# Optimization experiments

Measured on AMD Instinct MI355X. Metric: run time of the kernel, lower is better.

## Reference

```python
import jax, jax.numpy as jnp
import numpy as np

B, S, T = 4, 1024, 1024
HID, ATT, NH = 1024, 1024, 16
HD = ATT // NH  # head size 64


def setup_inputs() -> dict:
    key = jax.random.key(0)
    ks = jax.random.split(key, 12)
    sc = 1.0 / np.sqrt(HID)
    return {
        "src": jax.random.normal(ks[0], (B, S, HID), jnp.float32),
        "tgt": jax.random.normal(ks[1], (B, T, HID), jnp.float32),
        "src_mask": jax.random.randint(ks[2], (B, S), 0, 2) > 0,
        "tgt_mask": jax.random.randint(ks[3], (B, T), 0, 2) > 0,
        "qw": jax.random.normal(ks[4], (ATT, HID), jnp.float32) * sc,
        "qb": jnp.zeros((ATT,), jnp.float32),
        "kw": jax.random.normal(ks[5], (ATT, HID), jnp.float32) * sc,
        "kb": jnp.zeros((ATT,), jnp.float32),
        "vw": jax.random.normal(ks[6], (ATT, HID), jnp.float32) * sc,
        "vb": jnp.zeros((ATT,), jnp.float32),
        "ow": jax.random.normal(ks[7], (HID, ATT), jnp.float32) * (1.0 / np.sqrt(ATT)),
        "ob": jnp.zeros((HID,), jnp.float32),
    }


def _heads(x, w, b, L):
    # x:[B,L,HID] -> [B,NH,L,HD]
    return (x @ w.T + b).reshape(B, L, NH, HD).transpose(0, 2, 1, 3)


def reference(src, tgt, src_mask, tgt_mask, qw, qb, kw, kb, vw, vb, ow, ob):
    q = _heads(src, qw, qb, S)
    k = _heads(tgt, kw, kb, T)
    v_src = _heads(src, vw, vb, S)
    v_tgt = _heads(tgt, vw, vb, T)

    attn = jnp.einsum("bhsd,bhtd->bhst", q, k) / np.sqrt(HD)  # shared scores

    sm = src_mask[:, None, :, None].astype(attn.dtype)  # [B,1,S,1]
    tm = tgt_mask[:, None, None, :].astype(attn.dtype)  # [B,1,1,T]
    NEG = 100000.0
    attn_src = attn * sm - NEG * (1.0 - sm)
    attn_tgt = attn * tm - NEG * (1.0 - tm)

    p_src = jax.nn.softmax(attn_src, axis=-1)                        # [B,H,S,T]
    p_tgt = jax.nn.softmax(attn_tgt.swapaxes(-1, -2), axis=-1)       # [B,H,T,S]

    o_src = jnp.einsum("bhst,bhtd->bhsd", p_src, v_tgt)
    o_tgt = jnp.einsum("bhts,bhsd->bhtd", p_tgt, v_src)

    o_src = o_src.transpose(0, 2, 1, 3).reshape(B, S, ATT) @ ow.T + ob
    o_tgt = o_tgt.transpose(0, 2, 1, 3).reshape(B, T, ATT) @ ow.T + ob
    return (o_src, o_tgt)
```

## Files before the change

kernel.cpp:

```cpp
#include <hip/hip_runtime.h>
#include <stdint.h>

typedef _Float16 f16;
typedef _Float16 f16x8 __attribute__((ext_vector_type(8)));
typedef _Float16 f16x4 __attribute__((ext_vector_type(4)));
typedef float    f32x4 __attribute__((ext_vector_type(4)));

#define MFMA_F16(A, B, C) __builtin_amdgcn_mfma_f32_16x16x32_f16((A), (B), (C), 0, 0, 0)

__device__ __forceinline__ void gload_lds16(const void* g, void* l) {
  __builtin_amdgcn_global_load_lds((const __attribute__((address_space(1))) void*)g,
                                   (__attribute__((address_space(3))) void*)l, 16, 0, 0);
}

__global__ void cvt_f32_f16(const float* __restrict__ s0, const float* __restrict__ s1,
                            const float* __restrict__ s2, const float* __restrict__ s3,
                            const float* __restrict__ s4, const float* __restrict__ s5,
                            f16* __restrict__ d0, f16* __restrict__ d1, f16* __restrict__ d2,
                            f16* __restrict__ d3, f16* __restrict__ d4, f16* __restrict__ d5) {
  const float* sp; f16* dp; int n4;
  switch (blockIdx.y) {
    case 0:  sp = s0; dp = d0; n4 = (4096 * 1024) / 4; break;
    case 1:  sp = s1; dp = d1; n4 = (4096 * 1024) / 4; break;
    case 2:  sp = s2; dp = d2; n4 = (1024 * 1024) / 4; break;
    case 3:  sp = s3; dp = d3; n4 = (1024 * 1024) / 4; break;
    case 4:  sp = s4; dp = d4; n4 = (1024 * 1024) / 4; break;
    default: sp = s5; dp = d5; n4 = (1024 * 1024) / 4; break;
  }
  int stride = gridDim.x * blockDim.x;
  for (int i = blockIdx.x * blockDim.x + threadIdx.x; i < n4; i += stride) {
    f32x4 v = *(const f32x4*)(sp + (size_t)i * 4);
    f16x4 h;
    h[0] = (f16)v[0]; h[1] = (f16)v[1]; h[2] = (f16)v[2]; h[3] = (f16)v[3];
    *(f16x4*)(dp + (size_t)i * 4) = h;
  }
}

__device__ __forceinline__ void gemm_core_k1024(const f16* __restrict__ A, const f16* __restrict__ W,
                                                f16* lA, f16* lB, f32x4 (&acc)[4][4],
                                                int row0, int col0) {
  const int tid = threadIdx.x;
  const int lane = tid & 63;
  const int w = tid >> 6;
  const int g = lane >> 4, c = lane & 15;
  const int wr = (w >> 1) * 64, wc = (w & 1) * 64;

  int sr[2], scol[2];
#pragma unroll
  for (int p = 0; p < 2; ++p) {
    int slot = p * 256 + tid;
    int r = slot >> 2, sph = slot & 3;
    sr[p] = r;
    scol[p] = (sph ^ ((r >> 1) & 3)) * 8;
  }
  const f16* Abase = A + (size_t)row0 * 1024;
  const f16* Wbase = W + (size_t)col0 * 1024;

  for (int k0 = 0; k0 < 1024; k0 += 32) {
    __syncthreads();
#pragma unroll
    for (int p = 0; p < 2; ++p) {
      gload_lds16(Abase + (size_t)sr[p] * 1024 + k0 + scol[p], lA + (p * 256 + w * 64) * 8);
      gload_lds16(Wbase + (size_t)sr[p] * 1024 + k0 + scol[p], lB + (p * 256 + w * 64) * 8);
    }
    __syncthreads();
    f16x8 af[4], bf[4];
#pragma unroll
    for (int m = 0; m < 4; ++m) {
      int r = wr + m * 16 + c;
      af[m] = *(const f16x8*)(lA + r * 32 + (g ^ ((r >> 1) & 3)) * 8);
    }
#pragma unroll
    for (int n = 0; n < 4; ++n) {
      int r = wc + n * 16 + c;
      bf[n] = *(const f16x8*)(lB + r * 32 + (g ^ ((r >> 1) & 3)) * 8);
    }
#pragma unroll
    for (int m = 0; m < 4; ++m)
#pragma unroll
      for (int n = 0; n < 4; ++n)
        acc[m][n] = MFMA_F16(af[m], bf[n], acc[m][n]);
  }
}

__global__ __launch_bounds__(256, 2) void proj_gemm(
    const f16* __restrict__ src16, const f16* __restrict__ tgt16,
    const f16* __restrict__ qw16, const f16* __restrict__ kw16, const f16* __restrict__ vw16,
    const float* __restrict__ qb, const float* __restrict__ kb, const float* __restrict__ vb,
    f16* __restrict__ q16, f16* __restrict__ k16, f16* __restrict__ vtS, f16* __restrict__ vtT) {
  __shared__ f16 lA[128 * 32];
  __shared__ f16 lB[128 * 32];
  const int z = blockIdx.z;
  const f16* A = (z & 1) ? tgt16 : src16;
  const f16* W = (z == 0) ? qw16 : (z == 1) ? kw16 : vw16;
  const float* bias = (z == 0) ? qb : (z == 1) ? kb : vb;
  const int row0 = blockIdx.y * 128;
  const int col0 = blockIdx.x * 128;
  f32x4 acc[4][4] = {};
  gemm_core_k1024(A, W, lA, lB, acc, row0, col0);

  const int lane = threadIdx.x & 63;
  const int w = threadIdx.x >> 6;
  const int g = lane >> 4, c = lane & 15;
  const int wr = (w >> 1) * 64, wc = (w & 1) * 64;

  if (z < 2) {
    f16* O = (z == 0) ? q16 : k16;
#pragma unroll
    for (int n = 0; n < 4; ++n) {
      int colg = col0 + wc + n * 16 + c;
      float bv = bias[colg];
#pragma unroll
      for (int m = 0; m < 4; ++m) {
        int rb = row0 + wr + m * 16 + g * 4;
#pragma unroll
        for (int r = 0; r < 4; ++r)
          O[(size_t)(rb + r) * 1024 + colg] = (f16)(acc[m][n][r] + bv);
      }
    }
  } else {
    f16* O = (z == 2) ? vtS : vtT;
#pragma unroll
    for (int n = 0; n < 4; ++n) {
      int colg = col0 + wc + n * 16 + c;
      float bv = bias[colg];
#pragma unroll
      for (int m = 0; m < 4; ++m) {
        int row = row0 + wr + m * 16 + g * 4;
        int bb = row >> 10, t = row & 1023;
        int tl = t & 63;
        int tp = (t & ~63) + (tl & 32) + ((tl & 12) << 1) + ((tl & 16) >> 2) + (tl & 3);
        f16x4 pk;
#pragma unroll
        for (int r = 0; r < 4; ++r) pk[r] = (f16)(acc[m][n][r] + bv);
        *(f16x4*)(O + ((size_t)(bb << 10) + colg) * 1024 + tp) = pk;
      }
    }
  }
}

__global__ __launch_bounds__(256, 2) void out_gemm(
    const f16* __restrict__ opre, const f16* __restrict__ ow16,
    const float* __restrict__ ob, float* __restrict__ out) {
  __shared__ f16 lA[128 * 32];
  __shared__ f16 lB[128 * 32];
  const int row0 = blockIdx.y * 128;
  const int col0 = blockIdx.x * 128;
  f32x4 acc[4][4] = {};
  gemm_core_k1024(opre, ow16, lA, lB, acc, row0, col0);
  const int lane = threadIdx.x & 63;
  const int w = threadIdx.x >> 6;
  const int g = lane >> 4, c = lane & 15;
  const int wr = (w >> 1) * 64, wc = (w & 1) * 64;
#pragma unroll
  for (int n = 0; n < 4; ++n) {
    int colg = col0 + wc + n * 16 + c;
    float bv = ob[colg];
#pragma unroll
    for (int m = 0; m < 4; ++m) {
      int rb = row0 + wr + m * 16 + g * 4;
#pragma unroll
      for (int r = 0; r < 4; ++r)
        out[(size_t)(rb + r) * 1024 + colg] = acc[m][n][r] + bv;
    }
  }
}

__global__ __launch_bounds__(256, 3) void attn_fwd(
    const f16* __restrict__ q16, const f16* __restrict__ k16,
    const f16* __restrict__ vtS, const f16* __restrict__ vtT,
    const int* __restrict__ smask, const int* __restrict__ tmask,
    f16* __restrict__ opre) {
  const int bid = blockIdx.x;
  const int xcd = bid & 7;
  const int idx = bid >> 3;
  const int bhp = xcd * 16 + (idx >> 3);
  const int qblk = idx & 7;
  const int pass = bhp >> 6;
  const int bh = bhp & 63;
  const int b = bh >> 4, h = bh & 15;

  const f16* Q  = pass ? k16 : q16;
  const f16* Kt = pass ? q16 : k16;
  const f16* VT = pass ? vtS : vtT;
  const int* qmask = pass ? tmask : smask;
  const int outRowOff = pass ? 4096 : 0;

  const int tid = threadIdx.x;
  const int lane = tid & 63, wv = tid >> 6;
  const int g = lane >> 4, c = lane & 15;
  const int qrow0 = qblk * 128 + wv * 32;

  __shared__ f16 lK[2][64 * 64];
  __shared__ f16 lV[2][64 * 64];

  const size_t kbase = (size_t)b * (1024 * 1024) + h * 64;
  const size_t vbase = (size_t)bh * (64 * 1024);

  const float SC2 = 0.18033688f;
  f16x8 qf[2][2];
#pragma unroll
  for (int m = 0; m < 2; ++m) {
    f16 sh = (f16)(qmask[b * 1024 + qrow0 + m * 16 + c] ? SC2 : 0.0f);
#pragma unroll
    for (int kc = 0; kc < 2; ++kc) {
      f16x8 v = *(const f16x8*)(Q + ((size_t)(b * 1024 + qrow0 + m * 16 + c)) * 1024 + h * 64 + kc * 32 + g * 8);
#pragma unroll
      for (int j = 0; j < 8; ++j) v[j] *= sh;
      qf[m][kc] = v;
    }
  }

  auto STAGE = [&](int nb, int t0) {
#pragma unroll
    for (int i = 0; i < 2; ++i) {
      int p = i * 256 + tid;
      int row = p >> 3;
      int u = (p & 7) ^ (row & 7);
      gload_lds16(Kt + kbase + (size_t)(t0 + row) * 1024 + u * 8, &lK[nb][(i * 256 + wv * 64) * 8]);
      gload_lds16(VT + vbase + (size_t)row * 1024 + t0 + u * 8, &lV[nb][(i * 256 + wv * 64) * 8]);
    }
  };

  f32x4 accO[2][4] = {};
  float lpart[2] = {0.0f, 0.0f};

  STAGE(0, 0);

  for (int tt = 0; tt < 16; ++tt) {
    asm volatile("s_waitcnt vmcnt(0)" ::: "memory");
    __builtin_amdgcn_s_barrier();
    __builtin_amdgcn_sched_barrier(0);
    if (tt < 15) STAGE((tt + 1) & 1, (tt + 1) * 64);
    const f16* curK = lK[tt & 1];
    const f16* curV = lV[tt & 1];

    f16x8 kf[4][2];
#pragma unroll
    for (int n = 0; n < 4; ++n) {
      int row = n * 16 + c;
#pragma unroll
      for (int kc = 0; kc < 2; ++kc)
        kf[n][kc] = *(const f16x8*)(curK + row * 64 + (((kc * 4 + g) ^ (row & 7)) * 8));
    }

    f16x8 vf[4][2];
#pragma unroll
    for (int nd = 0; nd < 4; ++nd) {
      int row = nd * 16 + c;
#pragma unroll
      for (int kc = 0; kc < 2; ++kc)
        vf[nd][kc] = *(const f16x8*)(curV + row * 64 + (((kc * 4 + g) ^ (row & 7)) * 8));
    }

    f32x4 sc[2][4];
#pragma unroll
    for (int m = 0; m < 2; ++m)
#pragma unroll
      for (int n = 0; n < 4; ++n) {
        f32x4 z = {0.0f, 0.0f, 0.0f, 0.0f};
        z = MFMA_F16(kf[n][0], qf[m][0], z);
        sc[m][n] = MFMA_F16(kf[n][1], qf[m][1], z);
      }

    f16x8 pa[2][2];
#pragma unroll
    for (int m = 0; m < 2; ++m) {
      float e[16];
#pragma unroll
      for (int n = 0; n < 4; ++n)
#pragma unroll
        for (int r = 0; r < 4; ++r) e[n * 4 + r] = __builtin_amdgcn_exp2f(sc[m][n][r]);
      float s8[8];
#pragma unroll
      for (int i = 0; i < 8; ++i) s8[i] = e[i] + e[i + 8];
      float s4[4];
#pragma unroll
      for (int i = 0; i < 4; ++i) s4[i] = s8[i] + s8[i + 4];
      lpart[m] += (s4[0] + s4[1]) + (s4[2] + s4[3]);
#pragma unroll
      for (int kc = 0; kc < 2; ++kc) {
        f16x8 p8;
#pragma unroll
        for (int j = 0; j < 8; ++j) p8[j] = (f16)e[8 * kc + j];
        pa[m][kc] = p8;
      }
    }

#pragma unroll
    for (int m = 0; m < 2; ++m)
#pragma unroll
      for (int nd = 0; nd < 4; ++nd) {
        accO[m][nd] = MFMA_F16(pa[m][0], vf[nd][0], accO[m][nd]);
        accO[m][nd] = MFMA_F16(pa[m][1], vf[nd][1], accO[m][nd]);
      }
  }

#pragma unroll
  for (int m = 0; m < 2; ++m) {
    float ls = lpart[m];
    ls += __shfl_xor(ls, 16);
    ls += __shfl_xor(ls, 32);
#pragma unroll
    for (int r = 0; r < 4; ++r) {
      float lr = __shfl(ls, 20 * g + r);
      float inv = 1.0f / lr;
      size_t orow = (size_t)(outRowOff + b * 1024 + qrow0 + m * 16 + 4 * g + r);
#pragma unroll
      for (int nd = 0; nd < 4; ++nd)
        opre[orow * 1024 + h * 64 + nd * 16 + c] = (f16)(accO[m][nd][r] * inv);
    }
  }
}

extern "C" void kernel_launch(void* const* d_in, const int* in_sizes, int n_in,
                              void* d_out, int out_size, void* d_ws, size_t ws_size,
                              hipStream_t stream) {
  (void)in_sizes; (void)n_in; (void)out_size; (void)ws_size;
  const float* src = (const float*)d_in[0];
  const float* tgt = (const float*)d_in[1];
  const int*   smask = (const int*)d_in[2];
  const int*   tmask = (const int*)d_in[3];
  const float* qw = (const float*)d_in[4];
  const float* qb = (const float*)d_in[5];
  const float* kw = (const float*)d_in[6];
  const float* kb = (const float*)d_in[7];
  const float* vw = (const float*)d_in[8];
  const float* vb = (const float*)d_in[9];
  const float* ow = (const float*)d_in[10];
  const float* ob = (const float*)d_in[11];
  float* out = (float*)d_out;

  f16* wsp = (f16*)d_ws;
  const size_t M4 = (size_t)4096 * 1024;
  const size_t M1 = (size_t)1024 * 1024;
  f16* src16 = wsp;
  f16* tgt16 = src16 + M4;
  f16* qw16  = tgt16 + M4;
  f16* kw16  = qw16 + M1;
  f16* vw16  = kw16 + M1;
  f16* ow16  = vw16 + M1;
  f16* q16   = ow16 + M1;
  f16* k16   = q16 + M4;
  f16* vtS   = k16 + M4;
  f16* vtT   = vtS + M4;
  f16* opre  = wsp;

  cvt_f32_f16<<<dim3(512, 6), 256, 0, stream>>>(src, tgt, qw, kw, vw, ow,
                                                src16, tgt16, qw16, kw16, vw16, ow16);
  proj_gemm<<<dim3(8, 32, 4), 256, 0, stream>>>(src16, tgt16, qw16, kw16, vw16,
                                                qb, kb, vb, q16, k16, vtS, vtT);
  attn_fwd<<<dim3(1024), 256, 0, stream>>>(q16, k16, vtS, vtT, smask, tmask, opre);
  out_gemm<<<dim3(8, 64), 256, 0, stream>>>(opre, ow16, ob, out);
}
```

Before: 142.8 us.

## Double-buffer GEMM LDS tiles and remap blocks to XCDs for L2 reuse

The shared GEMM core now uses two LDS buffers and prefetches the next K tile while computing the current one, replacing the two-barrier-per-iteration single-buffer loop. The projection and output GEMMs switch to 1D grids whose block index is decoded so that blocks sharing an operand land on the same XCD, aiming for better L2 locality. This doubles LDS use per block, which may limit occupancy. The out_gemm mapping also carries dead, unused index computations.

After: 135.2 us. -5.3%, faster.

```diff
diff --git a/kernel.cpp b/kernel.cpp
--- a/kernel.cpp
+++ b/kernel.cpp
@@ -56,24 +56,37 @@
   const f16* Abase = A + (size_t)row0 * 1024;
   const f16* Wbase = W + (size_t)col0 * 1024;
 
-  for (int k0 = 0; k0 < 1024; k0 += 32) {
-    __syncthreads();
+  auto STAGE = [&](int nb, int k0) {
 #pragma unroll
     for (int p = 0; p < 2; ++p) {
-      gload_lds16(Abase + (size_t)sr[p] * 1024 + k0 + scol[p], lA + (p * 256 + w * 64) * 8);
-      gload_lds16(Wbase + (size_t)sr[p] * 1024 + k0 + scol[p], lB + (p * 256 + w * 64) * 8);
-    }
-    __syncthreads();
+      gload_lds16(Abase + (size_t)sr[p] * 1024 + k0 + scol[p],
+                  lA + nb * (128 * 32) + (p * 256 + w * 64) * 8);
+      gload_lds16(Wbase + (size_t)sr[p] * 1024 + k0 + scol[p],
+                  lB + nb * (128 * 32) + (p * 256 + w * 64) * 8);
+    }
+  };
+
+  STAGE(0, 0);
+
+  for (int kt = 0; kt < 32; ++kt) {
+    const int cur = kt & 1;
+    asm volatile("s_waitcnt vmcnt(0)" ::: "memory");
+    __builtin_amdgcn_s_barrier();
+    __builtin_amdgcn_sched_barrier(0);
+    if (kt < 31) STAGE(cur ^ 1, (kt + 1) * 32);
+
+    const f16* cA = lA + cur * (128 * 32);
+    const f16* cB = lB + cur * (128 * 32);
     f16x8 af[4], bf[4];
 #pragma unroll
     for (int m = 0; m < 4; ++m) {
       int r = wr + m * 16 + c;
-      af[m] = *(const f16x8*)(lA + r * 32 + (g ^ ((r >> 1) & 3)) * 8);
+      af[m] = *(const f16x8*)(cA + r * 32 + (g ^ ((r >> 1) & 3)) * 8);
     }
 #pragma unroll
     for (int n = 0; n < 4; ++n) {
       int r = wc + n * 16 + c;
-      bf[n] = *(const f16x8*)(lB + r * 32 + (g ^ ((r >> 1) & 3)) * 8);
+      bf[n] = *(const f16x8*)(cB + r * 32 + (g ^ ((r >> 1) & 3)) * 8);
     }
 #pragma unroll
     for (int m = 0; m < 4; ++m)
@@ -88,14 +101,20 @@
     const f16* __restrict__ qw16, const f16* __restrict__ kw16, const f16* __restrict__ vw16,
     const float* __restrict__ qb, const float* __restrict__ kb, const float* __restrict__ vb,
     f16* __restrict__ q16, f16* __restrict__ k16, f16* __restrict__ vtS, f16* __restrict__ vtT) {
-  __shared__ f16 lA[128 * 32];
-  __shared__ f16 lB[128 * 32];
-  const int z = blockIdx.z;
+  __shared__ f16 lA[2 * 128 * 32];
+  __shared__ f16 lB[2 * 128 * 32];
+  const int lin = blockIdx.x;
+  const int xcd = lin & 7;
+  const int slot = lin >> 3;
+  const int z = xcd >> 1;
+  const int y = (xcd & 1) * 16 + (slot >> 3);
+  const int x = slot & 7;
+
   const f16* A = (z & 1) ? tgt16 : src16;
   const f16* W = (z == 0) ? qw16 : (z == 1) ? kw16 : vw16;
   const float* bias = (z == 0) ? qb : (z == 1) ? kb : vb;
-  const int row0 = blockIdx.y * 128;
-  const int col0 = blockIdx.x * 128;
+  const int row0 = y * 128;
+  const int col0 = x * 128;
   f32x4 acc[4][4] = {};
   gemm_core_k1024(A, W, lA, lB, acc, row0, col0);
 
@@ -142,23 +161,43 @@
 __global__ __launch_bounds__(256, 2) void out_gemm(
     const f16* __restrict__ opre, const f16* __restrict__ ow16,
     const float* __restrict__ ob, float* __restrict__ out) {
-  __shared__ f16 lA[128 * 32];
-  __shared__ f16 lB[128 * 32];
-  const int row0 = blockIdx.y * 128;
-  const int col0 = blockIdx.x * 128;
+  __shared__ f16 lA[2 * 128 * 32];
+  __shared__ f16 lB[2 * 128 * 32];
+  const int lin = blockIdx.x;
+  const int xcd = lin & 7;
+  const int slot = lin >> 3;
+  const int y = xcd * 4 + (slot >> 2);
+  const int x = slot & 3;
+  const int row0 = y * 256;
+  (void)row0;
+  const int yy = xcd * 8 + (slot >> 1);
+  (void)yy;
+  const int Y = (lin >> 3);
+  (void)Y;
+  const int slot2 = lin >> 3;
+  const int y2 = xcd * 8 + (slot2 >> 2);
+  const int x2 = slot2 & 3;
+  const int r0 = y2 * 128;
+  const int c0 = x2 * 256;
+  const int slot3 = lin >> 3;
+  const int y3 = xcd * 8 + (slot3 >> 3);
+  const int x3 = slot3 & 7;
+  (void)r0; (void)c0; (void)x2; (void)y2; (void)slot2;
+  const int row_0 = y3 * 128;
+  const int col_0 = x3 * 128;
   f32x4 acc[4][4] = {};
-  gemm_core_k1024(opre, ow16, lA, lB, acc, row0, col0);
+  gemm_core_k1024(opre, ow16, lA, lB, acc, row_0, col_0);
   const int lane = threadIdx.x & 63;
   const int w = threadIdx.x >> 6;
   const int g = lane >> 4, c = lane & 15;
   const int wr = (w >> 1) * 64, wc = (w & 1) * 64;
 #pragma unroll
   for (int n = 0; n < 4; ++n) {
-    int colg = col0 + wc + n * 16 + c;
+    int colg = col_0 + wc + n * 16 + c;
     float bv = ob[colg];
 #pragma unroll
     for (int m = 0; m < 4; ++m) {
-      int rb = row0 + wr + m * 16 + g * 4;
+      int rb = row_0 + wr + m * 16 + g * 4;
 #pragma unroll
       for (int r = 0; r < 4; ++r)
         out[(size_t)(rb + r) * 1024 + colg] = acc[m][n][r] + bv;
@@ -348,8 +387,8 @@
 
   cvt_f32_f16<<<dim3(512, 6), 256, 0, stream>>>(src, tgt, qw, kw, vw, ow,
                                                 src16, tgt16, qw16, kw16, vw16, ow16);
-  proj_gemm<<<dim3(8, 32, 4), 256, 0, stream>>>(src16, tgt16, qw16, kw16, vw16,
-                                                qb, kb, vb, q16, k16, vtS, vtT);
+  proj_gemm<<<dim3(1024), 256, 0, stream>>>(src16, tgt16, qw16, kw16, vw16,
+                                            qb, kb, vb, q16, k16, vtS, vtT);
   attn_fwd<<<dim3(1024), 256, 0, stream>>>(q16, k16, vtS, vtT, smask, tmask, opre);
-  out_gemm<<<dim3(8, 64), 256, 0, stream>>>(opre, ow16, ob, out);
-}
+  out_gemm<<<dim3(512), 256, 0, stream>>>(opre, ow16, ob, out);
+}
```
